# Optimization experiments

Measured on AMD Instinct MI355X. Metric: run time of the kernel, lower is better.

The kernel has to match this reference:

```python
import jax, jax.numpy as jnp
import numpy as np

C = 256
NUM_HEADS = 4
GROUPS = 8
EPS = 1e-5


def setup_inputs() -> dict:
    key = jax.random.key(0)
    ks = jax.random.split(key, 8)
    N, H, W = 4, 64, 64
    x = jax.random.normal(ks[0], (N, C, H, W), dtype=jnp.float32)
    mask = jnp.ones((N, 1, H, W), dtype=jnp.float32)
    norm_w = jax.random.normal(ks[1], (C,), dtype=jnp.float32) * 0.02 + 1.0
    norm_b = jax.random.normal(ks[2], (C,), dtype=jnp.float32) * 0.02
    qkv_w = jax.random.normal(ks[3], (3 * C, C), dtype=jnp.float32) * (1.0 / np.sqrt(C))
    qkv_b = jax.random.normal(ks[4], (3 * C,), dtype=jnp.float32) * 0.02
    proj_w = jax.random.normal(ks[5], (C, C), dtype=jnp.float32) * (1.0 / np.sqrt(C))
    proj_b = jax.random.normal(ks[6], (C,), dtype=jnp.float32) * 0.02
    return {"x": x, "mask": mask, "norm_w": norm_w, "norm_b": norm_b,
            "qkv_w": qkv_w, "qkv_b": qkv_b, "proj_w": proj_w, "proj_b": proj_b}


def _group_norm(x, w, b):
    # x: [N, C, H, W]; normalize within GROUPS groups over (C//G, H, W)
    N, Cc, H, W = x.shape
    xg = x.reshape(N, GROUPS, Cc // GROUPS, H, W)
    mean = xg.mean(axis=(2, 3, 4), keepdims=True)
    var = xg.var(axis=(2, 3, 4), keepdims=True)
    xg = (xg - mean) * jax.lax.rsqrt(var + EPS)
    x = xg.reshape(N, Cc, H, W)
    return x * w[None, :, None, None] + b[None, :, None, None]


def reference(x, mask, norm_w, norm_b, qkv_w, qkv_b, proj_w, proj_b):
    N, Cc, H, W = x.shape
    h = NUM_HEADS
    hd = Cc // h  # head dim
    x_norm = _group_norm(x, norm_w, norm_b)
    # 1x1 conv == channel matmul: [N, 3C, H, W]
    qkv = jnp.einsum('nchw,oc->nohw', x_norm, qkv_w) + qkv_b[None, :, None, None]
    q, k, v = jnp.split(qkv, 3, axis=1)
    # n (h c) y x -> n h (y x) c
    def to_heads(t):
        return t.reshape(N, h, hd, H * W).transpose(0, 1, 3, 2)
    q, k, v = to_heads(q), to_heads(k), to_heads(v)
    scale = hd ** (-0.5)
    scores = jnp.einsum('nhic,nhjc->nhij', q, k) * scale  # [N,h,HW,HW]
    probs = jax.nn.softmax(scores, axis=-1)
    out = jnp.einsum('nhij,nhjc->nhic', probs, v)  # [N,h,HW,hd]
    # n h (y x) c -> n (h c) y x
    out = out.transpose(0, 1, 3, 2).reshape(N, Cc, H, W)
    out = jnp.einsum('nchw,oc->nohw', out, proj_w) + proj_b[None, :, None, None]
    y = (x + out) * mask[:, :1, :, :]  # broadcast over C (== repeat)
    return (y, mask)
```

## Files before the change

### kernel.cpp

```cpp
#include <hip/hip_runtime.h>

#define HW 4096
#define EPSV 1e-5f
#define SCL (0.125f * 1.44269504088896341f)

typedef unsigned short u16;
typedef unsigned int u32;
typedef __attribute__((ext_vector_type(8))) short short8;
typedef __attribute__((ext_vector_type(4))) short short4v;
typedef __attribute__((ext_vector_type(4))) float f32x4;

#define MFMA_K32(a, b, c) __builtin_amdgcn_mfma_f32_16x16x32_bf16((a), (b), (c), 0, 0, 0)
#if __has_builtin(__builtin_amdgcn_mfma_f32_16x16x16bf16_1k)
#define MFMA_K16(a, b, c) __builtin_amdgcn_mfma_f32_16x16x16bf16_1k((a), (b), (c), 0, 0, 0)
#elif __has_builtin(__builtin_amdgcn_mfma_f32_16x16x16_bf16)
#define MFMA_K16(a, b, c) __builtin_amdgcn_mfma_f32_16x16x16_bf16((a), (b), (c), 0, 0, 0)
#else
#define MFMA_K16(a, b, c) (c)
#endif

#define GLDS(g, l) __builtin_amdgcn_global_load_lds( \
    (const __attribute__((address_space(1))) u16*)(g), \
    (__attribute__((address_space(3))) u16*)(l), 16, 0, 0)

__device__ __forceinline__ u16 f2b(float f) {
    u32 u = __float_as_uint(f);
    u32 r = (u + 0x7FFFu + ((u >> 16) & 1u)) >> 16;
    return (u16)r;
}

__global__ __launch_bounds__(256) void gn_partial(const float* __restrict__ x, float* __restrict__ ps) {
    int bid = blockIdx.x;
    const float4* base = (const float4*)x + (size_t)bid * 2048;
    int t = threadIdx.x;
    float s = 0.f, sq = 0.f;
    for (int i = t; i < 2048; i += 256) {
        float4 v = base[i];
        s += v.x + v.y + v.z + v.w;
        sq += v.x * v.x + v.y * v.y + v.z * v.z + v.w * v.w;
    }
    __shared__ float rs[256], rq[256];
    rs[t] = s; rq[t] = sq;
    __syncthreads();
    for (int o = 128; o > 0; o >>= 1) {
        if (t < o) { rs[t] += rs[t + o]; rq[t] += rq[t + o]; }
        __syncthreads();
    }
    if (t == 0) { ps[2 * bid] = rs[0]; ps[2 * bid + 1] = rq[0]; }
}

__global__ __launch_bounds__(64) void gn_final(const float* __restrict__ ps, float* __restrict__ stats) {
    int t = threadIdx.x;
    if (t < 32) {
        float s = 0.f, sq = 0.f;
        for (int i = 0; i < 16; i++) {
            s += ps[2 * (t * 16 + i)];
            sq += ps[2 * (t * 16 + i) + 1];
        }
        float mean = s * (1.f / 131072.f);
        float var = sq * (1.f / 131072.f) - mean * mean;
        stats[t] = mean;
        stats[32 + t] = rsqrtf(var + EPSV);
    }
}

__global__ __launch_bounds__(256) void wconv(const float* __restrict__ src, u16* __restrict__ dst, int nscaled) {
    int idx = blockIdx.x * 256 + threadIdx.x;
    int row = idx >> 6;
    float sc = (row < nscaled) ? SCL : 1.0f;
    float4 v = *((const float4*)src + idx);
    u32 lo = (u32)f2b(v.x * sc) | ((u32)f2b(v.y * sc) << 16);
    u32 hi = (u32)f2b(v.z * sc) | ((u32)f2b(v.w * sc) << 16);
    uint2 o; o.x = lo; o.y = hi;
    *(uint2*)(dst + (size_t)idx * 4) = o;
}

__global__ __launch_bounds__(256) void gn_apply_t(const float* __restrict__ x, const float* __restrict__ w,
                                                  const float* __restrict__ b, const float* __restrict__ stats,
                                                  u16* __restrict__ xt) {
    __shared__ u16 Tt[64][72];
    int t = threadIdx.x;
    int p0 = blockIdx.x * 64;
    int c0 = blockIdx.y * 64;
    int n = blockIdx.z;
    int pc = (t & 15) * 4;
#pragma unroll
    for (int jj = 0; jj < 4; jj++) {
        int r = (t >> 4) + jj * 16;
        int c = c0 + r;
        int grp = n * 8 + (c >> 5);
        float mean = stats[grp], rstd = stats[32 + grp];
        float a = rstd * w[c];
        float bb = b[c] - mean * a;
        float4 v = *(const float4*)(x + ((size_t)n * 256 + c) * HW + p0 + pc);
        Tt[pc + 0][r] = f2b(v.x * a + bb);
        Tt[pc + 1][r] = f2b(v.y * a + bb);
        Tt[pc + 2][r] = f2b(v.z * a + bb);
        Tt[pc + 3][r] = f2b(v.w * a + bb);
    }
    __syncthreads();
    int p = t >> 2, ck = t & 3;
    short8 s0 = *(const short8*)&Tt[p][ck * 16];
    short8 s1 = *(const short8*)&Tt[p][ck * 16 + 8];
    u16* dst = xt + ((size_t)n * HW + p0 + p) * 256 + c0 + ck * 16;
    *(short8*)dst = s0;
    *(short8*)(dst + 8) = s1;
}

__global__ __launch_bounds__(256) void qkv_mfma(const u16* __restrict__ xt, const u16* __restrict__ Wb,
                                                const float* __restrict__ bq, u16* __restrict__ Qw,
                                                u16* __restrict__ Kw, u16* __restrict__ Vw) {
    __shared__ u16 Xs[64 * 256];
    int t = threadIdx.x;
    int w = t >> 6, lane = t & 63;
    int col = lane & 15, quad = lane >> 4;
    int p0 = blockIdx.x * 64;
    int o0 = blockIdx.y * 64;
    int n = blockIdx.z;

#pragma unroll
    for (int j = 0; j < 8; j++) {
        int rl = j * 2 + (lane >> 5);
        int row = w * 16 + rl;
        int slot = (lane & 31) ^ (rl & 7);
        GLDS(xt + ((size_t)n * HW + p0 + row) * 256 + slot * 8, Xs + (w * 16 + j * 2) * 256);
    }

    const u16* wrow = Wb + (size_t)(o0 + w * 16 + col) * 256 + quad * 8;
    short8 A[8];
#pragma unroll
    for (int ks = 0; ks < 8; ks++) A[ks] = *(const short8*)(wrow + ks * 32);

    __syncthreads();

    f32x4 C[4];
#pragma unroll
    for (int pb = 0; pb < 4; pb++) C[pb] = (f32x4){0.f, 0.f, 0.f, 0.f};
    int c7 = col & 7;
#pragma unroll
    for (int pb = 0; pb < 4; pb++) {
        const u16* xr = Xs + (pb * 16 + col) * 256;
#pragma unroll
        for (int ks = 0; ks < 8; ks++) {
            int slot = (ks * 4 + quad) ^ c7;
            short8 Bf = *(const short8*)(xr + slot * 8);
            C[pb] = MFMA_K32(A[ks], Bf, C[pb]);
        }
    }

    int type = o0 >> 8;
    int h = (o0 >> 6) & 3;
    int nh = n * 4 + h;
    float sc = (type == 0) ? SCL : 1.0f;
    if (type == 2) {
#pragma unroll
        for (int rg = 0; rg < 4; rg++) {
            int d = w * 16 + quad * 4 + rg;
            float bias = bq[o0 + d];
            u16* vb = Vw + ((size_t)nh * 64 + d) * HW + p0 + col;
#pragma unroll
            for (int pb = 0; pb < 4; pb++)
                vb[pb * 16] = f2b(C[pb][rg] + bias);
        }
    } else {
        u16* dst = (type == 0 ? Qw : Kw) + ((size_t)nh * HW + p0 + col) * 64 + w * 16 + quad * 4;
        float b0 = sc * bq[o0 + w * 16 + quad * 4 + 0];
        float b1 = sc * bq[o0 + w * 16 + quad * 4 + 1];
        float b2 = sc * bq[o0 + w * 16 + quad * 4 + 2];
        float b3 = sc * bq[o0 + w * 16 + quad * 4 + 3];
#pragma unroll
        for (int pb = 0; pb < 4; pb++) {
            uint2 o;
            o.x = (u32)f2b(C[pb][0] + b0) | ((u32)f2b(C[pb][1] + b1) << 16);
            o.y = (u32)f2b(C[pb][2] + b2) | ((u32)f2b(C[pb][3] + b3) << 16);
            *(uint2*)(dst + (size_t)(pb * 16) * 64) = o;
        }
    }
}

__global__ __launch_bounds__(256) void flash_mfma(const u16* __restrict__ Qw, const u16* __restrict__ Kw,
                                                  const u16* __restrict__ Vw, u16* __restrict__ attnT) {
    __shared__ u16 Ks[2][128 * 64];
    __shared__ u16 Vts[2][64 * 128];
    int t = threadIdx.x;
    int w = t >> 6, lane = t & 63;
    int col = lane & 15, quad = lane >> 4;
    int q0 = blockIdx.x * 128;
    int nh = blockIdx.y;

    const u16* qp = Qw + ((size_t)nh * HW + q0 + w * 32 + col) * 64 + quad * 8;
    short8 qa0 = *(const short8*)qp;
    short8 qa1 = *(const short8*)(qp + 32);
    short8 qc0 = *(const short8*)(qp + 1024);
    short8 qc1 = *(const short8*)(qp + 1024 + 32);

    f32x4 OaA[4], OaB[4];
#pragma unroll
    for (int db = 0; db < 4; db++) {
        OaA[db] = (f32x4){0.f, 0.f, 0.f, 0.f};
        OaB[db] = (f32x4){0.f, 0.f, 0.f, 0.f};
    }
    float lA = 0.f, lB = 0.f;

    const u16* kbase = Kw + (size_t)nh * HW * 64;
    const u16* vbase = Vw + (size_t)nh * 64 * HW;
    int lrK = lane >> 3;
    int ccK = lane & 7;
    size_t kSrc = (size_t)(w * 8 + lrK) * 64 + (ccK ^ lrK) * 8;
    int rvV = lane >> 4;
    int cvV = lane & 15;

#define STAGE(jt_, b_) do { \
        int j0_ = (jt_) * 128; \
        _Pragma("unroll") \
        for (int s_ = 0; s_ < 4; s_++) \
            GLDS(kbase + (size_t)j0_ * 64 + kSrc + (size_t)(s_ * 32) * 64, &Ks[b_][(w * 8 + s_ * 32) * 64]); \
        _Pragma("unroll") \
        for (int m_ = 0; m_ < 4; m_++) { \
            int d_ = w * 16 + m_ * 4 + rvV; \
            GLDS(vbase + (size_t)d_ * HW + j0_ + ((cvV ^ (d_ & 7)) * 8), &Vts[b_][(w * 16 + m_ * 4) * 128]); \
        } \
    } while (0)

    STAGE(0, 0);
    __syncthreads();

    int c7 = col & 7;
    for (int jt = 0; jt < 32; jt++) {
        int cur = jt & 1;
        if (jt < 31) STAGE(jt + 1, cur ^ 1);
        const u16* KsC = Ks[cur];
        const u16* VtC = Vts[cur];

        f32x4 sA[8], sB[8];
#pragma unroll
        for (int jb = 0; jb < 8; jb++) {
            const u16* kr = KsC + (jb * 16 + col) * 64;
            short8 ka0 = *(const short8*)(kr + ((quad ^ c7) * 8));
            short8 ka1 = *(const short8*)(kr + (((quad + 4) ^ c7) * 8));
            f32x4 a = (f32x4){0.f, 0.f, 0.f, 0.f};
            a = MFMA_K32(ka0, qa0, a);
            a = MFMA_K32(ka1, qa1, a);
            sA[jb] = a;
            f32x4 b = (f32x4){0.f, 0.f, 0.f, 0.f};
            b = MFMA_K32(ka0, qc0, b);
            b = MFMA_K32(ka1, qc1, b);
            sB[jb] = b;
        }

        short4v ptA[8], ptB[8];
        float lpA = 0.f, lpB = 0.f;
#pragma unroll
        for (int jb = 0; jb < 8; jb++) {
#pragma unroll
            for (int rg = 0; rg < 4; rg++) {
                float pa = __builtin_amdgcn_exp2f(sA[jb][rg]);
                float pb = __builtin_amdgcn_exp2f(sB[jb][rg]);
                lpA += pa; lpB += pb;
                ptA[jb][rg] = (short)(__float_as_uint(pa) >> 16);
                ptB[jb][rg] = (short)(__float_as_uint(pb) >> 16);
            }
        }
        lA += lpA;
        lB += lpB;

#pragma unroll
        for (int db = 0; db < 4; db++) {
            const u16* vr = VtC + (db * 16 + col) * 128;
#pragma unroll
            for (int jb = 0; jb < 8; jb++) {
                int ch = jb * 2 + (quad >> 1);
                short4v va = *(const short4v*)(vr + ((ch ^ c7) * 8) + (quad & 1) * 4);
                OaA[db] = MFMA_K16(va, ptA[jb], OaA[db]);
                OaB[db] = MFMA_K16(va, ptB[jb], OaB[db]);
            }
        }
        __syncthreads();
    }
#undef STAGE

    lA += __shfl_xor(lA, 16);
    lB += __shfl_xor(lB, 16);
    lA += __shfl_xor(lA, 32);
    lB += __shfl_xor(lB, 32);

    float rlA = 1.0f / lA, rlB = 1.0f / lB;
    u16* abA = attnT + ((size_t)(nh >> 2) * HW + q0 + w * 32 + col) * 256 + (nh & 3) * 64 + quad * 4;
    u16* abB = abA + 16 * 256;
#pragma unroll
    for (int db = 0; db < 4; db++) {
        uint2 oA, oB;
        oA.x = (u32)f2b(OaA[db][0] * rlA) | ((u32)f2b(OaA[db][1] * rlA) << 16);
        oA.y = (u32)f2b(OaA[db][2] * rlA) | ((u32)f2b(OaA[db][3] * rlA) << 16);
        oB.x = (u32)f2b(OaB[db][0] * rlB) | ((u32)f2b(OaB[db][1] * rlB) << 16);
        oB.y = (u32)f2b(OaB[db][2] * rlB) | ((u32)f2b(OaB[db][3] * rlB) << 16);
        *(uint2*)(abA + db * 16) = oA;
        *(uint2*)(abB + db * 16) = oB;
    }
}

__global__ __launch_bounds__(256) void proj_mfma(const u16* __restrict__ attnT, const u16* __restrict__ Wpb,
                                                 const float* __restrict__ bp, const float* __restrict__ x,
                                                 const float* __restrict__ mask, float* __restrict__ out) {
    __shared__ u16 Xs[64 * 256];
    int t = threadIdx.x;
    int w = t >> 6, lane = t & 63;
    int col = lane & 15, quad = lane >> 4;
    int p0 = blockIdx.x * 64;
    int o0 = blockIdx.y * 64;
    int n = blockIdx.z;

#pragma unroll
    for (int j = 0; j < 8; j++) {
        int rl = j * 2 + (lane >> 5);
        int row = w * 16 + rl;
        int slot = (lane & 31) ^ (rl & 7);
        GLDS(attnT + ((size_t)n * HW + p0 + row) * 256 + slot * 8, Xs + (w * 16 + j * 2) * 256);
    }

    const u16* wrow = Wpb + (size_t)(o0 + w * 16 + col) * 256 + quad * 8;
    short8 A[8];
#pragma unroll
    for (int ks = 0; ks < 8; ks++) A[ks] = *(const short8*)(wrow + ks * 32);

    __syncthreads();

    f32x4 C[4];
#pragma unroll
    for (int pb = 0; pb < 4; pb++) C[pb] = (f32x4){0.f, 0.f, 0.f, 0.f};
    int c7 = col & 7;
#pragma unroll
    for (int pb = 0; pb < 4; pb++) {
        const u16* xr = Xs + (pb * 16 + col) * 256;
#pragma unroll
        for (int ks = 0; ks < 8; ks++) {
            int slot = (ks * 4 + quad) ^ c7;
            short8 Bf = *(const short8*)(xr + slot * 8);
            C[pb] = MFMA_K32(A[ks], Bf, C[pb]);
        }
    }

#pragma unroll
    for (int rg = 0; rg < 4; rg++) {
        int o = o0 + w * 16 + quad * 4 + rg;
        float bias = bp[o];
        const float* xb = x + ((size_t)n * 256 + o) * HW + p0 + col;
        float* ob = out + ((size_t)n * 256 + o) * HW + p0 + col;
        const float* mb = mask + (size_t)n * HW + p0 + col;
#pragma unroll
        for (int pb = 0; pb < 4; pb++) {
            float mv = mb[pb * 16];
            ob[pb * 16] = (xb[pb * 16] + C[pb][rg] + bias) * mv;
        }
    }
}

__global__ __launch_bounds__(256) void mask_copy(const float* __restrict__ mask, float* __restrict__ out) {
    int i = blockIdx.x * 256 + threadIdx.x;
    out[i] = mask[i];
}

extern "C" void kernel_launch(void* const* d_in, const int* in_sizes, int n_in,
                              void* d_out, int out_size, void* d_ws, size_t ws_size,
                              hipStream_t stream) {
    const float* x = (const float*)d_in[0];
    const float* mask = (const float*)d_in[1];
    const float* norm_w = (const float*)d_in[2];
    const float* norm_b = (const float*)d_in[3];
    const float* qkv_w = (const float*)d_in[4];
    const float* qkv_b = (const float*)d_in[5];
    const float* proj_w = (const float*)d_in[6];
    const float* proj_b = (const float*)d_in[7];
    float* out = (float*)d_out;

    float* ws = (float*)d_ws;
    float* stats = ws;
    float* pstats = ws + 64;
    u16* xt = (u16*)(ws + 2048);
    u16* Qw = xt + 4194304;
    u16* Kw = Qw + 4194304;
    u16* Vw = Kw + 4194304;
    u16* attnT = Vw + 4194304;
    u16* Wqb = attnT + 4194304;
    u16* Wpb = Wqb + 196608;

    gn_partial<<<512, 256, 0, stream>>>(x, pstats);
    gn_final<<<1, 64, 0, stream>>>(pstats, stats);
    wconv<<<192, 256, 0, stream>>>(qkv_w, Wqb, 256);
    wconv<<<64, 256, 0, stream>>>(proj_w, Wpb, 0);
    gn_apply_t<<<dim3(64, 4, 4), 256, 0, stream>>>(x, norm_w, norm_b, stats, xt);
    qkv_mfma<<<dim3(64, 12, 4), 256, 0, stream>>>(xt, Wqb, qkv_b, Qw, Kw, Vw);
    flash_mfma<<<dim3(32, 16), 256, 0, stream>>>(Qw, Kw, Vw, attnT);
    proj_mfma<<<dim3(64, 4, 4), 256, 0, stream>>>(attnT, Wpb, proj_b, x, mask, out);
    mask_copy<<<64, 256, 0, stream>>>(mask, out + 4194304);
}
```

Measured before the change: 218.0 us.

## Split flash attention KV range across two wave groups and merge via LDS

The flash attention kernel now launches 512 threads per block, with two halves of 4 waves each processing disjoint halves of the key/value sequence using 64-wide tiles. Their partial outputs and row sums are combined through shared memory at the end. Row sums are now computed with an MFMA against a ones vector instead of scalar adds, and the bf16 conversion of probabilities uses rounding plus byte permutes. The aim is to raise wave occupancy and latency hiding across a grid of only 512 blocks, at the cost of a final LDS merge and synchronization.

```diff
diff --git a/kernel.cpp b/kernel.cpp
--- a/kernel.cpp
+++ b/kernel.cpp
@@ -178,17 +178,18 @@
     }
 }
 
-__global__ __launch_bounds__(256) void flash_mfma(const u16* __restrict__ Qw, const u16* __restrict__ Kw,
-                                                  const u16* __restrict__ Vw, u16* __restrict__ attnT) {
-    __shared__ u16 Ks[2][128 * 64];
-    __shared__ u16 Vts[2][64 * 128];
+__global__ __launch_bounds__(512, 4) void flash_mfma(const u16* __restrict__ Qw, const u16* __restrict__ Kw,
+                                                     const u16* __restrict__ Vw, u16* __restrict__ attnT) {
+    __shared__ u16 Ks[4][64 * 64];
+    __shared__ u16 Vts[4][64 * 64];
     int t = threadIdx.x;
     int w = t >> 6, lane = t & 63;
+    int half = w >> 2, wl = w & 3;
     int col = lane & 15, quad = lane >> 4;
     int q0 = blockIdx.x * 128;
     int nh = blockIdx.y;
 
-    const u16* qp = Qw + ((size_t)nh * HW + q0 + w * 32 + col) * 64 + quad * 8;
+    const u16* qp = Qw + ((size_t)nh * HW + q0 + wl * 32 + col) * 64 + quad * 8;
     short8 qa0 = *(const short8*)qp;
     short8 qa1 = *(const short8*)(qp + 32);
     short8 qc0 = *(const short8*)(qp + 1024);
@@ -200,25 +201,25 @@
         OaA[db] = (f32x4){0.f, 0.f, 0.f, 0.f};
         OaB[db] = (f32x4){0.f, 0.f, 0.f, 0.f};
     }
-    float lA = 0.f, lB = 0.f;
+    f32x4 lacA = (f32x4){0.f, 0.f, 0.f, 0.f};
+    f32x4 lacB = (f32x4){0.f, 0.f, 0.f, 0.f};
 
     const u16* kbase = Kw + (size_t)nh * HW * 64;
     const u16* vbase = Vw + (size_t)nh * 64 * HW;
     int lrK = lane >> 3;
     int ccK = lane & 7;
-    size_t kSrc = (size_t)(w * 8 + lrK) * 64 + (ccK ^ lrK) * 8;
-    int rvV = lane >> 4;
-    int cvV = lane & 15;
+    size_t kSrc = (size_t)(wl * 8 + lrK) * 64 + (ccK ^ lrK) * 8;
+    int jbase = half * 2048;
 
 #define STAGE(jt_, b_) do { \
-        int j0_ = (jt_) * 128; \
+        int j0_ = jbase + (jt_) * 64; \
         _Pragma("unroll") \
-        for (int s_ = 0; s_ < 4; s_++) \
-            GLDS(kbase + (size_t)j0_ * 64 + kSrc + (size_t)(s_ * 32) * 64, &Ks[b_][(w * 8 + s_ * 32) * 64]); \
+        for (int s_ = 0; s_ < 2; s_++) \
+            GLDS(kbase + (size_t)j0_ * 64 + kSrc + (size_t)(s_ * 32) * 64, &Ks[half * 2 + (b_)][(wl * 8 + s_ * 32) * 64]); \
         _Pragma("unroll") \
-        for (int m_ = 0; m_ < 4; m_++) { \
-            int d_ = w * 16 + m_ * 4 + rvV; \
-            GLDS(vbase + (size_t)d_ * HW + j0_ + ((cvV ^ (d_ & 7)) * 8), &Vts[b_][(w * 16 + m_ * 4) * 128]); \
+        for (int s_ = 0; s_ < 2; s_++) { \
+            int d_ = wl * 8 + s_ * 32 + lrK; \
+            GLDS(vbase + (size_t)d_ * HW + j0_ + ((ccK ^ lrK) * 8), &Vts[half * 2 + (b_)][(wl * 8 + s_ * 32) * 64]); \
         } \
     } while (0)
 
@@ -226,15 +227,16 @@
     __syncthreads();
 
     int c7 = col & 7;
+    const short4v ones = {0x3F80, 0x3F80, 0x3F80, 0x3F80};
     for (int jt = 0; jt < 32; jt++) {
         int cur = jt & 1;
         if (jt < 31) STAGE(jt + 1, cur ^ 1);
-        const u16* KsC = Ks[cur];
-        const u16* VtC = Vts[cur];
-
-        f32x4 sA[8], sB[8];
-#pragma unroll
-        for (int jb = 0; jb < 8; jb++) {
+        const u16* KsC = Ks[half * 2 + cur];
+        const u16* VtC = Vts[half * 2 + cur];
+
+        f32x4 sA[4], sB[4];
+#pragma unroll
+        for (int jb = 0; jb < 4; jb++) {
             const u16* kr = KsC + (jb * 16 + col) * 64;
             short8 ka0 = *(const short8*)(kr + ((quad ^ c7) * 8));
             short8 ka1 = *(const short8*)(kr + (((quad + 4) ^ c7) * 8));
@@ -248,27 +250,35 @@
             sB[jb] = b;
         }
 
-        short4v ptA[8], ptB[8];
-        float lpA = 0.f, lpB = 0.f;
-#pragma unroll
-        for (int jb = 0; jb < 8; jb++) {
+        short4v ptA[4], ptB[4];
+#pragma unroll
+        for (int jb = 0; jb < 4; jb++) {
+            u32 ua[4], ub[4];
 #pragma unroll
             for (int rg = 0; rg < 4; rg++) {
-                float pa = __builtin_amdgcn_exp2f(sA[jb][rg]);
-                float pb = __builtin_amdgcn_exp2f(sB[jb][rg]);
-                lpA += pa; lpB += pb;
-                ptA[jb][rg] = (short)(__float_as_uint(pa) >> 16);
-                ptB[jb][rg] = (short)(__float_as_uint(pb) >> 16);
+                ua[rg] = __float_as_uint(__builtin_amdgcn_exp2f(sA[jb][rg])) + 0x8000u;
+                ub[rg] = __float_as_uint(__builtin_amdgcn_exp2f(sB[jb][rg])) + 0x8000u;
             }
-        }
-        lA += lpA;
-        lB += lpB;
+            uint2 pa2, pb2;
+            pa2.x = __builtin_amdgcn_perm(ua[1], ua[0], 0x07060302u);
+            pa2.y = __builtin_amdgcn_perm(ua[3], ua[2], 0x07060302u);
+            pb2.x = __builtin_amdgcn_perm(ub[1], ub[0], 0x07060302u);
+            pb2.y = __builtin_amdgcn_perm(ub[3], ub[2], 0x07060302u);
+            ptA[jb] = __builtin_bit_cast(short4v, pa2);
+            ptB[jb] = __builtin_bit_cast(short4v, pb2);
+        }
+
+#pragma unroll
+        for (int jb = 0; jb < 4; jb++) {
+            lacA = MFMA_K16(ones, ptA[jb], lacA);
+            lacB = MFMA_K16(ones, ptB[jb], lacB);
+        }
 
 #pragma unroll
         for (int db = 0; db < 4; db++) {
-            const u16* vr = VtC + (db * 16 + col) * 128;
-#pragma unroll
-            for (int jb = 0; jb < 8; jb++) {
+            const u16* vr = VtC + (db * 16 + col) * 64;
+#pragma unroll
+            for (int jb = 0; jb < 4; jb++) {
                 int ch = jb * 2 + (quad >> 1);
                 short4v va = *(const short4v*)(vr + ((ch ^ c7) * 8) + (quad & 1) * 4);
                 OaA[db] = MFMA_K16(va, ptA[jb], OaA[db]);
@@ -279,23 +289,46 @@
     }
 #undef STAGE
 
-    lA += __shfl_xor(lA, 16);
-    lB += __shfl_xor(lB, 16);
-    lA += __shfl_xor(lA, 32);
-    lB += __shfl_xor(lB, 32);
-
-    float rlA = 1.0f / lA, rlB = 1.0f / lB;
-    u16* abA = attnT + ((size_t)(nh >> 2) * HW + q0 + w * 32 + col) * 256 + (nh & 3) * 64 + quad * 4;
-    u16* abB = abA + 16 * 256;
-#pragma unroll
-    for (int db = 0; db < 4; db++) {
-        uint2 oA, oB;
-        oA.x = (u32)f2b(OaA[db][0] * rlA) | ((u32)f2b(OaA[db][1] * rlA) << 16);
-        oA.y = (u32)f2b(OaA[db][2] * rlA) | ((u32)f2b(OaA[db][3] * rlA) << 16);
-        oB.x = (u32)f2b(OaB[db][0] * rlB) | ((u32)f2b(OaB[db][1] * rlB) << 16);
-        oB.y = (u32)f2b(OaB[db][2] * rlB) | ((u32)f2b(OaB[db][3] * rlB) << 16);
-        *(uint2*)(abA + db * 16) = oA;
-        *(uint2*)(abB + db * 16) = oB;
+    float* mO = (float*)&Ks[0][0];
+    float* mL = (float*)&Vts[0][0];
+    int widx = wl * 64 + lane;
+    if (half == 1) {
+#pragma unroll
+        for (int db = 0; db < 4; db++) {
+#pragma unroll
+            for (int rg = 0; rg < 4; rg++) {
+                mO[(db * 8 + rg) * 256 + widx] = OaA[db][rg];
+                mO[(db * 8 + 4 + rg) * 256 + widx] = OaB[db][rg];
+            }
+        }
+        mL[widx] = lacA[0];
+        mL[256 + widx] = lacB[0];
+    }
+    __syncthreads();
+    if (half == 0) {
+        float lA = lacA[0] + mL[widx];
+        float lB = lacB[0] + mL[256 + widx];
+        float rlA = 1.0f / lA, rlB = 1.0f / lB;
+        u16* abA = attnT + ((size_t)(nh >> 2) * HW + q0 + wl * 32 + col) * 256 + (nh & 3) * 64 + quad * 4;
+        u16* abB = abA + 16 * 256;
+#pragma unroll
+        for (int db = 0; db < 4; db++) {
+            float a0 = OaA[db][0] + mO[(db * 8 + 0) * 256 + widx];
+            float a1 = OaA[db][1] + mO[(db * 8 + 1) * 256 + widx];
+            float a2 = OaA[db][2] + mO[(db * 8 + 2) * 256 + widx];
+            float a3 = OaA[db][3] + mO[(db * 8 + 3) * 256 + widx];
+            float b0 = OaB[db][0] + mO[(db * 8 + 4) * 256 + widx];
+            float b1 = OaB[db][1] + mO[(db * 8 + 5) * 256 + widx];
+            float b2 = OaB[db][2] + mO[(db * 8 + 6) * 256 + widx];
+            float b3 = OaB[db][3] + mO[(db * 8 + 7) * 256 + widx];
+            uint2 oA, oB;
+            oA.x = (u32)f2b(a0 * rlA) | ((u32)f2b(a1 * rlA) << 16);
+            oA.y = (u32)f2b(a2 * rlA) | ((u32)f2b(a3 * rlA) << 16);
+            oB.x = (u32)f2b(b0 * rlB) | ((u32)f2b(b1 * rlB) << 16);
+            oB.y = (u32)f2b(b2 * rlB) | ((u32)f2b(b3 * rlB) << 16);
+            *(uint2*)(abA + db * 16) = oA;
+            *(uint2*)(abB + db * 16) = oB;
+        }
     }
 }
 
@@ -390,7 +423,7 @@
     wconv<<<64, 256, 0, stream>>>(proj_w, Wpb, 0);
     gn_apply_t<<<dim3(64, 4, 4), 256, 0, stream>>>(x, norm_w, norm_b, stats, xt);
     qkv_mfma<<<dim3(64, 12, 4), 256, 0, stream>>>(xt, Wqb, qkv_b, Qw, Kw, Vw);
-    flash_mfma<<<dim3(32, 16), 256, 0, stream>>>(Qw, Kw, Vw, attnT);
+    flash_mfma<<<dim3(32, 16), 512, 0, stream>>>(Qw, Kw, Vw, attnT);
     proj_mfma<<<dim3(64, 4, 4), 256, 0, stream>>>(attnT, Wpb, proj_b, x, mask, out);
     mask_copy<<<64, 256, 0, stream>>>(mask, out + 4194304);
 }
```

Measured after the change: 211.0 us. 1.03x faster.
